# Kernel tuning notes

Hardware: AMD Instinct MI355X
Metric: run time of the kernel (lower is better)

Reference implementation:

```python
import jax, jax.numpy as jnp
import numpy as np

LEVELS = [(128, 128), (64, 64), (32, 32), (16, 16)]  # (H, W) per level
B, D, NH, NL, NP, DFF, NLAYERS = 2, 256, 8, 4, 4, 1024, 6
DH = D // NH
Q = sum(h * w for h, w in LEVELS)


def setup_inputs() -> dict:
    key = jax.random.key(0)
    ks = iter(jax.random.split(key, 64))
    inp = {}
    for i, (h, w) in enumerate(LEVELS):
        inp[f"src{i}"] = jax.random.normal(next(ks), (B, D, h, w), jnp.float32)
        inp[f"pos{i}"] = jax.random.normal(next(ks), (B, D, h, w), jnp.float32) * 0.1
    s = 0.02
    def p(shape):
        return jax.random.normal(next(ks), shape, jnp.float32) * s
    inp["level_embed"] = p((NL, D))
    inp["W_off"] = p((NLAYERS, D, NH * NL * NP * 2)); inp["b_off"] = p((NLAYERS, NH * NL * NP * 2))
    inp["W_aw"] = p((NLAYERS, D, NH * NL * NP)); inp["b_aw"] = p((NLAYERS, NH * NL * NP))
    inp["W_v"] = p((NLAYERS, D, D)); inp["b_v"] = p((NLAYERS, D))
    inp["W_out"] = p((NLAYERS, D, D)); inp["b_out"] = p((NLAYERS, D))
    inp["g1"] = jnp.ones((NLAYERS, D)); inp["be1"] = jnp.zeros((NLAYERS, D))
    inp["W1"] = p((NLAYERS, D, DFF)); inp["b1"] = p((NLAYERS, DFF))
    inp["W2"] = p((NLAYERS, DFF, D)); inp["b2"] = p((NLAYERS, D))
    inp["g2"] = jnp.ones((NLAYERS, D)); inp["be2"] = jnp.zeros((NLAYERS, D))
    return inp


def layer_norm(x, g, b, eps=1e-5):
    m = x.mean(-1, keepdims=True)
    v = ((x - m) ** 2).mean(-1, keepdims=True)
    return (x - m) * jax.lax.rsqrt(v + eps) * g + b


def bilinear_sample(v, loc, H, W):
    # v: [B,NH,H*W,DH], loc: [B,NH,Q,NP,2] normalized to [0,1] (grid_sample, align_corners=False, zero pad)
    x = loc[..., 0] * W - 0.5
    y = loc[..., 1] * H - 0.5
    x0f = jnp.floor(x); y0f = jnp.floor(y)
    wx = (x - x0f)[..., None]; wy = (y - y0f)[..., None]
    x0 = x0f.astype(jnp.int32); y0 = y0f.astype(jnp.int32)
    def gather(xi, yi):
        ok = ((xi >= 0) & (xi < W) & (yi >= 0) & (yi < H))[..., None]
        idx = jnp.clip(yi, 0, H - 1) * W + jnp.clip(xi, 0, W - 1)
        b, h, q, pp = idx.shape
        g = jnp.take_along_axis(v, idx.reshape(b, h, q * pp, 1), axis=2).reshape(b, h, q, pp, -1)
        return jnp.where(ok, g, jnp.zeros((), v.dtype))
    v00 = gather(x0, y0); v10 = gather(x0 + 1, y0)
    v01 = gather(x0, y0 + 1); v11 = gather(x0 + 1, y0 + 1)
    return (v00 * (1 - wx) * (1 - wy) + v10 * wx * (1 - wy)
            + v01 * (1 - wx) * wy + v11 * wx * wy)


def deform_attn(x, q, ref, wh, Woff, boff, Waw, baw, Wv, bv, Wout, bout):
    off = (q @ Woff + boff).reshape(B, Q, NH, NL, NP, 2)
    aw = jax.nn.softmax((q @ Waw + baw).reshape(B, Q, NH, NL * NP), -1).reshape(B, Q, NH, NL, NP)
    v = (x @ Wv + bv).reshape(B, Q, NH, DH)
    # sampling locations: [B,Q,NH,NL,NP,2]
    loc = ref[:, :, None, :, None, :] + off / wh[None, None, None, :, None, :]
    out = jnp.zeros((B, Q, NH, DH), x.dtype)
    start = 0
    for lvl, (h, w) in enumerate(LEVELS):
        n = h * w
        vl = v[:, start:start + n].transpose(0, 2, 1, 3)          # [B,NH,n,DH]
        locl = loc[:, :, :, lvl].transpose(0, 2, 1, 3, 4)          # [B,NH,Q,NP,2]
        sampled = bilinear_sample(vl, locl, h, w)                  # [B,NH,Q,NP,DH]
        out = out + jnp.einsum('bqhp,bhqpd->bqhd', aw[:, :, :, lvl], sampled)
        start += n
    return out.reshape(B, Q, D) @ Wout + bout


def _ref_points():
    refs = []
    for h, w in LEVELS:
        ry, rx = jnp.meshgrid(jnp.linspace(0.5, h - 0.5, h) / h,
                              jnp.linspace(0.5, w - 0.5, w) / w, indexing='ij')
        refs.append(jnp.stack([rx.reshape(-1), ry.reshape(-1)], -1))
    r = jnp.concatenate(refs, 0)                                   # [Q,2]
    return jnp.broadcast_to(r[None, :, None, :], (B, Q, NL, 2))    # valid_ratios == 1


def reference(src0, src1, src2, src3, pos0, pos1, pos2, pos3, level_embed,
              W_off, b_off, W_aw, b_aw, W_v, b_v, W_out, b_out,
              g1, be1, W1, b1, W2, b2, g2, be2):
    srcs = [src0, src1, src2, src3]
    poss = [pos0, pos1, pos2, pos3]
    x = jnp.concatenate([s.reshape(B, D, -1).transpose(0, 2, 1) for s in srcs], 1)
    pos = jnp.concatenate([p.reshape(B, D, -1).transpose(0, 2, 1) + level_embed[i][None, None]
                           for i, p in enumerate(poss)], 1)
    ref = _ref_points()
    wh = jnp.array([[w, h] for h, w in LEVELS], jnp.float32)       # offset normalizer (W,H)
    for l in range(NLAYERS):
        q = x + pos
        attn = deform_attn(x, q, ref, wh, W_off[l], b_off[l], W_aw[l], b_aw[l],
                           W_v[l], b_v[l], W_out[l], b_out[l])
        x = layer_norm(x + attn, g1[l], be1[l])
        f = jax.nn.relu(x @ W1[l] + b1[l]) @ W2[l] + b2[l]
        x = layer_norm(x + f, g2[l], be2[l])
    spatial_shapes = jnp.array(LEVELS, jnp.int32)
    sizes = np.array([h * w for h, w in LEVELS])
    level_start_index = jnp.array(np.concatenate([[0], np.cumsum(sizes)[:-1]]), jnp.int32)
    return (x, spatial_shapes, level_start_index)
```

## Files before the change

### kernel.cpp

```cpp
#include <hip/hip_runtime.h>
#include <cstddef>

#define BB 2
#define DD 256
#define NH 8
#define NL 4
#define NP 4
#define DFF 1024
#define NLAYERS 6
#define Q_TOT 21760
#define NTOK (BB * Q_TOT)
#define MTILES (NTOK / 128)
#define LTILES (NTOK / 64)

typedef unsigned short ushort_t;
typedef __attribute__((ext_vector_type(8))) short bh8;
typedef __attribute__((ext_vector_type(4))) float fx4;

__device__ __forceinline__ ushort_t f2b(float x) {
  union { float f; unsigned u; } v; v.f = x;
  unsigned r = v.u + 0x7FFF + ((v.u >> 16) & 1);
  return (ushort_t)(r >> 16);
}
__device__ __forceinline__ float b2f(ushort_t b) {
  union { unsigned u; float f; } v; v.u = ((unsigned)b) << 16; return v.f;
}
__device__ __forceinline__ float b2f_hi(unsigned w) {
  union { unsigned u; float f; } v; v.u = w & 0xFFFF0000u; return v.f;
}
__device__ __forceinline__ float b2f_lo(unsigned w) {
  union { unsigned u; float f; } v; v.u = w << 16; return v.f;
}

__device__ __forceinline__ void gload16(const void* g, void* l) {
  __builtin_amdgcn_global_load_lds(
      (const __attribute__((address_space(1))) unsigned int*)g,
      (__attribute__((address_space(3))) unsigned int*)l, 16, 0, 0);
}

__global__ __launch_bounds__(256) void flatten_level(
    const float* __restrict__ src, const float* __restrict__ pos,
    const float* __restrict__ lemb, float* __restrict__ X,
    ushort_t* __restrict__ Xb, ushort_t* __restrict__ POSb,
    ushort_t* __restrict__ QBb, int HW, int start, int lvl) {
  __shared__ float ts[32][33];
  __shared__ float tp[32][33];
  int p0 = blockIdx.x * 32, d0 = blockIdx.y * 32, b = blockIdx.z;
  const float* sb = src + (size_t)b * DD * HW;
  const float* pb = pos + (size_t)b * DD * HW;
  int px = threadIdx.x;
#pragma unroll
  for (int i = 0; i < 4; ++i) {
    int dl = threadIdx.y + i * 8;
    ts[dl][px] = sb[(size_t)(d0 + dl) * HW + p0 + px];
    tp[dl][px] = pb[(size_t)(d0 + dl) * HW + p0 + px];
  }
  __syncthreads();
  int dx = threadIdx.x;
#pragma unroll
  for (int i = 0; i < 4; ++i) {
    int pl = threadIdx.y + i * 8;
    size_t row = (size_t)b * Q_TOT + start + p0 + pl;
    float s = ts[dx][pl];
    float p = tp[dx][pl] + lemb[lvl * DD + d0 + dx];
    X[row * DD + d0 + dx] = s;
    Xb[row * DD + d0 + dx] = f2b(s);
    POSb[row * DD + d0 + dx] = f2b(p);
    QBb[row * DD + d0 + dx] = f2b(s + p);
  }
}

__global__ __launch_bounds__(256) void transpose_w(const float* __restrict__ W,
                                                   ushort_t* __restrict__ WT,
                                                   int K, int N, int outStride,
                                                   int rowOff) {
  __shared__ float t[32][33];
  int n0 = blockIdx.x * 32, k0 = blockIdx.y * 32, l = blockIdx.z;
  const float* in = W + (size_t)l * K * N;
  ushort_t* out = WT + (size_t)l * outStride;
#pragma unroll
  for (int i = 0; i < 4; ++i) {
    int k = threadIdx.y + i * 8;
    t[k][threadIdx.x] = in[(size_t)(k0 + k) * N + n0 + threadIdx.x];
  }
  __syncthreads();
#pragma unroll
  for (int i = 0; i < 4; ++i) {
    int nn = threadIdx.y + i * 8;
    out[(size_t)(rowOff + n0 + nn) * K + k0 + threadIdx.x] = f2b(t[threadIdx.x][nn]);
  }
}

__global__ void pack_bias(const float* __restrict__ b_off,
                          const float* __restrict__ b_aw,
                          float* __restrict__ b_qa) {
  int l = blockIdx.x, i = threadIdx.x;
  b_qa[l * 384 + i] = (i < 256) ? b_off[l * 256 + i] : b_aw[l * 128 + i - 256];
}

template <int RELU, int OUTBF16>
__global__ __launch_bounds__(256) void gemm_mfma(
    const ushort_t* __restrict__ A, const ushort_t* __restrict__ Bt,
    const float* __restrict__ bias, void* __restrict__ C, int N, int K) {
  __shared__ ushort_t As[128 * 64];
  __shared__ ushort_t Bs[128 * 64];
  int tid = threadIdx.x;
  int m0 = blockIdx.y * 128, n0 = blockIdx.x * 128;
  int wid = tid >> 6, lane = tid & 63;
  int wr = wid >> 1, wc = wid & 1;

  fx4 acc[4][4];
#pragma unroll
  for (int i = 0; i < 4; ++i)
#pragma unroll
    for (int j = 0; j < 4; ++j) acc[i][j] = fx4{0.f, 0.f, 0.f, 0.f};

  const ushort_t* ga = A + (size_t)(m0 + (tid >> 3)) * K + (tid & 7) * 8;
  const ushort_t* gb = Bt + (size_t)(n0 + (tid >> 3)) * K + (tid & 7) * 8;
  int ldsbase = wid * 1024;

  for (int k0 = 0; k0 < K; k0 += 64) {
#pragma unroll
    for (int it = 0; it < 4; ++it) {
      gload16(ga + (size_t)(it * 32) * K + k0, (char*)As + ldsbase + it * 4096);
      gload16(gb + (size_t)(it * 32) * K + k0, (char*)Bs + ldsbase + it * 4096);
    }
    __syncthreads();
#pragma unroll
    for (int kk = 0; kk < 2; ++kk) {
      bh8 af[4], bf[4];
      int cb = kk * 64 + (lane >> 4) * 16;
      int ra = wr * 64 + (lane & 15);
      int rb = wc * 64 + (lane & 15);
#pragma unroll
      for (int i = 0; i < 4; ++i)
        af[i] = *(const bh8*)((const char*)As + (ra + i * 16) * 128 + cb);
#pragma unroll
      for (int i = 0; i < 4; ++i)
        bf[i] = *(const bh8*)((const char*)Bs + (rb + i * 16) * 128 + cb);
#pragma unroll
      for (int i = 0; i < 4; ++i)
#pragma unroll
        for (int j = 0; j < 4; ++j)
          acc[i][j] = __builtin_amdgcn_mfma_f32_16x16x32_bf16(af[i], bf[j], acc[i][j], 0, 0, 0);
    }
    __syncthreads();
  }

  int crow = m0 + wr * 64 + (lane >> 4) * 4;
  int ccol = n0 + wc * 64 + (lane & 15);
#pragma unroll
  for (int j = 0; j < 4; ++j) {
    float bv = bias[ccol + j * 16];
#pragma unroll
    for (int i = 0; i < 4; ++i) {
#pragma unroll
      for (int r = 0; r < 4; ++r) {
        float v = acc[i][j][r] + bv;
        if (RELU) v = fmaxf(v, 0.f);
        size_t idx = (size_t)(crow + i * 16 + r) * N + ccol + j * 16;
        if (OUTBF16) ((ushort_t*)C)[idx] = f2b(v);
        else ((float*)C)[idx] = v;
      }
    }
  }
}

__global__ __launch_bounds__(256) void gemm_ln(
    const ushort_t* __restrict__ A, const ushort_t* __restrict__ Bt,
    const float* __restrict__ bias, const float* __restrict__ gamma,
    const float* __restrict__ beta, ushort_t* __restrict__ Xbio, int K) {
  __shared__ ushort_t As[2][64 * 32];
  __shared__ ushort_t Bs[2][256 * 32];
  __shared__ float red[2][2][64];
  int tid = threadIdx.x;
  int m0 = blockIdx.x * 64;
  int wid = tid >> 6, lane = tid & 63;
  int wr = wid >> 1, wc = wid & 1;

  fx4 acc[2][8];
#pragma unroll
  for (int i = 0; i < 2; ++i)
#pragma unroll
    for (int j = 0; j < 8; ++j) acc[i][j] = fx4{0.f, 0.f, 0.f, 0.f};

  int srow = tid >> 2;
  int sslot = (tid & 3) ^ ((tid >> 3) & 3);
  const ushort_t* ga = A + (size_t)(m0 + srow) * K + sslot * 8;
  const ushort_t* gb = Bt + (size_t)srow * K + sslot * 8;
  int ldsoff = wid * 1024;

  int cbyte = (((lane >> 4) ^ ((lane >> 1) & 3)) << 4);
  int ra = wr * 32 + (lane & 15);
  int rb = wc * 128 + (lane & 15);

  gload16(ga, (char*)As[0] + ldsoff);
#pragma unroll
  for (int it = 0; it < 4; ++it)
    gload16(gb + (size_t)(it * 64) * K, (char*)Bs[0] + it * 4096 + ldsoff);
  __syncthreads();

  int nt = K >> 5;
  int cur = 0;
  for (int t = 0; t < nt; ++t) {
    if (t + 1 < nt) {
      int k1 = (t + 1) << 5;
      gload16(ga + k1, (char*)As[cur ^ 1] + ldsoff);
#pragma unroll
      for (int it = 0; it < 4; ++it)
        gload16(gb + (size_t)(it * 64) * K + k1, (char*)Bs[cur ^ 1] + it * 4096 + ldsoff);
    }
    bh8 af[2], bf[8];
#pragma unroll
    for (int i = 0; i < 2; ++i)
      af[i] = *(const bh8*)((const char*)As[cur] + (ra + i * 16) * 64 + cbyte);
#pragma unroll
    for (int j = 0; j < 8; ++j)
      bf[j] = *(const bh8*)((const char*)Bs[cur] + (rb + j * 16) * 64 + cbyte);
#pragma unroll
    for (int i = 0; i < 2; ++i)
#pragma unroll
      for (int j = 0; j < 8; ++j)
        acc[i][j] = __builtin_amdgcn_mfma_f32_16x16x32_bf16(af[i], bf[j], acc[i][j], 0, 0, 0);
    __syncthreads();
    cur ^= 1;
  }

  int lg = lane >> 4, lc = lane & 15;
  float bv[8], gv[8], bev[8];
#pragma unroll
  for (int j = 0; j < 8; ++j) {
    int col = wc * 128 + j * 16 + lc;
    bv[j] = bias[col];
    gv[j] = gamma[col];
    bev[j] = beta[col];
  }
#pragma unroll
  for (int i = 0; i < 2; ++i) {
#pragma unroll
    for (int r = 0; r < 4; ++r) {
      int rloc = wr * 32 + i * 16 + lg * 4 + r;
      const ushort_t* xr = Xbio + (size_t)(m0 + rloc) * DD + wc * 128 + lc;
      float s = 0.f, s2 = 0.f;
#pragma unroll
      for (int j = 0; j < 8; ++j) {
        float v = acc[i][j][r] + bv[j] + b2f(xr[j * 16]);
        acc[i][j][r] = v;
        s += v;
        s2 += v * v;
      }
#pragma unroll
      for (int o = 1; o < 16; o <<= 1) {
        s += __shfl_xor(s, o);
        s2 += __shfl_xor(s2, o);
      }
      if (lc == 0) {
        red[wc][0][rloc] = s;
        red[wc][1][rloc] = s2;
      }
    }
  }
  __syncthreads();
#pragma unroll
  for (int i = 0; i < 2; ++i) {
#pragma unroll
    for (int r = 0; r < 4; ++r) {
      int rloc = wr * 32 + i * 16 + lg * 4 + r;
      float s = red[0][0][rloc] + red[1][0][rloc];
      float s2 = red[0][1][rloc] + red[1][1][rloc];
      float mmean = s * (1.f / 256.f);
      float var = s2 * (1.f / 256.f) - mmean * mmean;
      float inv = rsqrtf(var + 1e-5f);
      size_t rowb = (size_t)(m0 + rloc) * DD + wc * 128 + lc;
#pragma unroll
      for (int j = 0; j < 8; ++j) {
        float y = (acc[i][j][r] - mmean) * inv * gv[j] + bev[j];
        Xbio[rowb + j * 16] = f2b(y);
      }
    }
  }
}

template <int LAST>
__global__ __launch_bounds__(512, 2) void ffn_fused(
    const ushort_t* __restrict__ Xio, const ushort_t* __restrict__ W1t,
    const float* __restrict__ b1v, const ushort_t* __restrict__ W2t,
    const float* __restrict__ b2v, const float* __restrict__ gamma,
    const float* __restrict__ beta, const ushort_t* __restrict__ POSb,
    ushort_t* __restrict__ QBb, float* __restrict__ Xf) {
  extern __shared__ char lds[];
  int tid = threadIdx.x;
  int w = tid >> 6, l = tid & 63;
  int l15 = l & 15, l4 = l >> 4, l7 = l & 7;
  int m0 = blockIdx.x * 64;

  fx4 acc[4][8];
#pragma unroll
  for (int i = 0; i < 4; ++i)
#pragma unroll
    for (int j = 0; j < 8; ++j) acc[i][j] = fx4{0.f, 0.f, 0.f, 0.f};

  const ushort_t* xb = Xio + (size_t)m0 * 256;
#pragma unroll
  for (int kk = 0; kk < 8; ++kk) {
    bh8 af[4], bf[8];
#pragma unroll
    for (int i = 0; i < 4; ++i)
      af[i] = *(const bh8*)(xb + (size_t)(l15 + 16 * i) * 256 + kk * 32 + l4 * 8);
#pragma unroll
    for (int j = 0; j < 8; ++j)
      bf[j] = *(const bh8*)(W1t + (size_t)(w * 128 + j * 16 + l15) * 256 + kk * 32 + l4 * 8);
#pragma unroll
    for (int i = 0; i < 4; ++i)
#pragma unroll
      for (int j = 0; j < 8; ++j)
        acc[i][j] = __builtin_amdgcn_mfma_f32_16x16x32_bf16(af[i], bf[j], acc[i][j], 0, 0, 0);
  }
#pragma unroll
  for (int j = 0; j < 8; ++j) {
    int n = w * 128 + j * 16 + l15;
    float bb = b1v[n];
    int slotbase = n >> 3;
    int nlo = (n & 7) * 2;
#pragma unroll
    for (int i = 0; i < 4; ++i) {
#pragma unroll
      for (int r = 0; r < 4; ++r) {
        int m = l4 * 4 + r + 16 * i;
        float h = fmaxf(acc[i][j][r] + bb, 0.f);
        *(ushort_t*)(lds + m * 2048 + ((slotbase ^ (m & 7)) << 4) + nlo) = f2b(h);
      }
    }
  }
  __syncthreads();

  fx4 acc2[4][2];
#pragma unroll
  for (int i = 0; i < 4; ++i)
#pragma unroll
    for (int j = 0; j < 2; ++j) acc2[i][j] = fx4{0.f, 0.f, 0.f, 0.f};

#pragma unroll 4
  for (int kt = 0; kt < 32; ++kt) {
    bh8 af[4], bf[2];
#pragma unroll
    for (int i = 0; i < 4; ++i) {
      int m = l15 + 16 * i;
      af[i] = *(const bh8*)(lds + m * 2048 + (((kt * 4 + l4) ^ l7) << 4));
    }
#pragma unroll
    for (int j = 0; j < 2; ++j)
      bf[j] = *(const bh8*)(W2t + (size_t)(w * 32 + j * 16 + l15) * 1024 + kt * 32 + l4 * 8);
#pragma unroll
    for (int i = 0; i < 4; ++i)
#pragma unroll
      for (int j = 0; j < 2; ++j)
        acc2[i][j] = __builtin_amdgcn_mfma_f32_16x16x32_bf16(af[i], bf[j], acc2[i][j], 0, 0, 0);
  }
  __syncthreads();

  float* red = (float*)lds;
  float* minv = (float*)(lds + 4096);

  float gv[2], bev[2], bv2[2];
#pragma unroll
  for (int j = 0; j < 2; ++j) {
    int col = w * 32 + j * 16 + l15;
    gv[j] = gamma[col];
    bev[j] = beta[col];
    bv2[j] = b2v[col];
  }
#pragma unroll
  for (int i = 0; i < 4; ++i) {
#pragma unroll
    for (int r = 0; r < 4; ++r) {
      int m = l4 * 4 + r + 16 * i;
      float s = 0.f, s2 = 0.f;
#pragma unroll
      for (int j = 0; j < 2; ++j) {
        int col = w * 32 + j * 16 + l15;
        float v = acc2[i][j][r] + bv2[j] + b2f(Xio[(size_t)(m0 + m) * 256 + col]);
        acc2[i][j][r] = v;
        s += v;
        s2 += v * v;
      }
#pragma unroll
      for (int o = 1; o < 16; o <<= 1) {
        s += __shfl_xor(s, o);
        s2 += __shfl_xor(s2, o);
      }
      if (l15 == 0) {
        red[w * 64 + m] = s;
        red[512 + w * 64 + m] = s2;
      }
    }
  }
  __syncthreads();
  if (tid < 64) {
    float s = 0.f, s2 = 0.f;
#pragma unroll
    for (int ww = 0; ww < 8; ++ww) {
      s += red[ww * 64 + tid];
      s2 += red[512 + ww * 64 + tid];
    }
    float mean = s * (1.f / 256.f);
    float var = s2 * (1.f / 256.f) - mean * mean;
    minv[tid * 2] = mean;
    minv[tid * 2 + 1] = rsqrtf(var + 1e-5f);
  }
  __syncthreads();
  ushort_t* XbOut = (ushort_t*)Xio;
#pragma unroll
  for (int i = 0; i < 4; ++i) {
#pragma unroll
    for (int r = 0; r < 4; ++r) {
      int m = l4 * 4 + r + 16 * i;
      float mean = minv[m * 2], inv = minv[m * 2 + 1];
      size_t rowb = (size_t)(m0 + m) * 256;
#pragma unroll
      for (int j = 0; j < 2; ++j) {
        int col = w * 32 + j * 16 + l15;
        float y = (acc2[i][j][r] - mean) * inv * gv[j] + bev[j];
        XbOut[rowb + col] = f2b(y);
        if (LAST) Xf[rowb + col] = y;
        else QBb[rowb + col] = f2b(y + b2f(POSb[rowb + col]));
      }
    }
  }
}

__global__ __launch_bounds__(256) void sample_v4(const ushort_t* __restrict__ Vb,
                                                 const ushort_t* __restrict__ QA,
                                                 ushort_t* __restrict__ SAMPb) {
  int nb = NTOK / 2;
  int bid = blockIdx.x;
  int newb = (bid & 7) * (nb >> 3) + (bid >> 3);
  int t = newb * 2 + (threadIdx.x >> 7);
  int h = (threadIdx.x >> 4) & 7;
  int p = threadIdx.x & 15;

  int b = (t >= Q_TOT) ? 1 : 0;
  int qi = t - b * Q_TOT;
  int lwq = (qi < 16384) ? 7 : (qi < 20480) ? 6 : (qi < 21504) ? 5 : 4;
  int stq = (qi < 16384) ? 0 : (qi < 20480) ? 16384 : (qi < 21504) ? 20480 : 21504;
  int wt = 1 << lwq;
  int pidx = qi - stq;
  int iy = pidx >> lwq, ix = pidx & (wt - 1);
  float refx = (ix + 0.5f) / (float)wt;
  float refy = (iy + 0.5f) / (float)wt;

  float lgt = b2f(QA[(size_t)t * 384 + 256 + h * 16 + p]);
  float mxv = lgt;
#pragma unroll
  for (int o = 1; o < 16; o <<= 1) mxv = fmaxf(mxv, __shfl_xor(mxv, o, 16));
  float e = __expf(lgt - mxv);
  float sum = e;
#pragma unroll
  for (int o = 1; o < 16; o <<= 1) sum += __shfl_xor(sum, o, 16);
  float a = e / sum;

  int l = p >> 2, pt = p & 3;
  int wl = 128 >> l;
  int LSl = (l > 0 ? 16384 : 0) + (l > 1 ? 4096 : 0) + (l > 2 ? 1024 : 0);
  float fw = (float)wl;
  unsigned ow = *(const unsigned*)(QA + (size_t)t * 384 + h * 32 + l * 8 + pt * 2);
  float ox = b2f_lo(ow), oy = b2f_hi(ow);
  float Xc = refx * fw + ox - 0.5f;
  float Yc = refy * fw + oy - 0.5f;
  float xf = floorf(Xc), yf = floorf(Yc);
  float wx = Xc - xf, wy = Yc - yf;
  int x0 = (int)xf, y0 = (int)yf;
  int x1 = x0 + 1, y1 = y0 + 1;
  float ok_x0 = (x0 >= 0 && x0 < wl) ? 1.f : 0.f;
  float ok_x1 = (x1 >= 0 && x1 < wl) ? 1.f : 0.f;
  float ok_y0 = (y0 >= 0 && y0 < wl) ? 1.f : 0.f;
  float ok_y1 = (y1 >= 0 && y1 < wl) ? 1.f : 0.f;
  int xc0 = min(max(x0, 0), wl - 1), xc1 = min(max(x1, 0), wl - 1);
  int yc0 = min(max(y0, 0), wl - 1), yc1 = min(max(y1, 0), wl - 1);
  float w00 = (1.f - wx) * (1.f - wy) * a * ok_x0 * ok_y0;
  float w10 = wx * (1.f - wy) * a * ok_x1 * ok_y0;
  float w01 = (1.f - wx) * wy * a * ok_x0 * ok_y1;
  float w11 = wx * wy * a * ok_x1 * ok_y1;
  int metaBase = ((b * Q_TOT + LSl + yc0 * wl + xc0) << 8) + h * 32;
  int metaDxy = (int)(((unsigned)((xc1 - xc0) << 8)) |
                      (((unsigned)((yc1 - yc0) * wl) << 8) << 16));
  int metaZ = (int)(((unsigned)f2b(w00) << 16) | f2b(w10));
  int metaW = (int)(((unsigned)f2b(w01) << 16) | f2b(w11));

  int c2 = p * 2;
  float acc0 = 0.f, acc1 = 0.f;
#pragma unroll
  for (int pp = 0; pp < 16; ++pp) {
    int m0v = __shfl(metaBase, pp, 16);
    int m1v = __shfl(metaDxy, pp, 16);
    int mzv = __shfl(metaZ, pp, 16);
    int mwv = __shfl(metaW, pp, 16);
    unsigned dxy = (unsigned)m1v;
    int base = m0v + c2;
    int dx = (int)(dxy & 0xffffu);
    int dy = (int)(dxy >> 16);
    unsigned v00 = *(const unsigned*)(Vb + base);
    unsigned v10 = *(const unsigned*)(Vb + base + dx);
    unsigned v01 = *(const unsigned*)(Vb + base + dy);
    unsigned v11 = *(const unsigned*)(Vb + base + dy + dx);
    unsigned wz = (unsigned)mzv, ww = (unsigned)mwv;
    float f00 = b2f_hi(wz), f10 = b2f_lo(wz);
    float f01 = b2f_hi(ww), f11 = b2f_lo(ww);
    acc0 = fmaf(f00, b2f_lo(v00), acc0);
    acc1 = fmaf(f00, b2f_hi(v00), acc1);
    acc0 = fmaf(f10, b2f_lo(v10), acc0);
    acc1 = fmaf(f10, b2f_hi(v10), acc1);
    acc0 = fmaf(f01, b2f_lo(v01), acc0);
    acc1 = fmaf(f01, b2f_hi(v01), acc1);
    acc0 = fmaf(f11, b2f_lo(v11), acc0);
    acc1 = fmaf(f11, b2f_hi(v11), acc1);
  }
  unsigned outw = (unsigned)f2b(acc0) | ((unsigned)f2b(acc1) << 16);
  *(unsigned*)(SAMPb + (size_t)t * 256 + h * 32 + c2) = outw;
}

__global__ void write_tail(float* __restrict__ t) {
  int i = threadIdx.x;
  float v = 0.f;
  switch (i) {
    case 0: v = 128.f; break;
    case 1: v = 128.f; break;
    case 2: v = 64.f; break;
    case 3: v = 64.f; break;
    case 4: v = 32.f; break;
    case 5: v = 32.f; break;
    case 6: v = 16.f; break;
    case 7: v = 16.f; break;
    case 8: v = 0.f; break;
    case 9: v = 16384.f; break;
    case 10: v = 20480.f; break;
    case 11: v = 21504.f; break;
    default: return;
  }
  t[i] = v;
}

extern "C" void kernel_launch(void* const* d_in, const int* in_sizes, int n_in,
                              void* d_out, int out_size, void* d_ws, size_t ws_size,
                              hipStream_t stream) {
  const float* src[4] = {(const float*)d_in[0], (const float*)d_in[2],
                         (const float*)d_in[4], (const float*)d_in[6]};
  const float* pos[4] = {(const float*)d_in[1], (const float*)d_in[3],
                         (const float*)d_in[5], (const float*)d_in[7]};
  const float* lemb = (const float*)d_in[8];
  const float* W_off = (const float*)d_in[9];
  const float* b_off = (const float*)d_in[10];
  const float* W_aw = (const float*)d_in[11];
  const float* b_aw = (const float*)d_in[12];
  const float* W_v = (const float*)d_in[13];
  const float* b_v = (const float*)d_in[14];
  const float* W_out = (const float*)d_in[15];
  const float* b_out = (const float*)d_in[16];
  const float* g1 = (const float*)d_in[17];
  const float* be1 = (const float*)d_in[18];
  const float* W1 = (const float*)d_in[19];
  const float* b1 = (const float*)d_in[20];
  const float* W2 = (const float*)d_in[21];
  const float* b2 = (const float*)d_in[22];
  const float* g2 = (const float*)d_in[23];
  const float* be2 = (const float*)d_in[24];

  float* X = (float*)d_out;

  char* w = (char*)d_ws;
  const size_t SZ_B = (size_t)NTOK * 256 * 2;
  ushort_t* POSb = (ushort_t*)w;  w += SZ_B;
  ushort_t* Xb = (ushort_t*)w;    w += SZ_B;
  ushort_t* QBb = (ushort_t*)w;   w += SZ_B;
  ushort_t* QAb = (ushort_t*)w;   w += (size_t)NTOK * 384 * 2;
  ushort_t* Vb = (ushort_t*)w;    w += SZ_B;
  ushort_t* SAMPb = (ushort_t*)w; w += SZ_B;
  ushort_t* WT_qa = (ushort_t*)w;  w += (size_t)NLAYERS * 384 * 256 * 2;
  ushort_t* WT_v = (ushort_t*)w;   w += (size_t)NLAYERS * 256 * 256 * 2;
  ushort_t* WT_out = (ushort_t*)w; w += (size_t)NLAYERS * 256 * 256 * 2;
  ushort_t* WT_1 = (ushort_t*)w;   w += (size_t)NLAYERS * 1024 * 256 * 2;
  ushort_t* WT_2 = (ushort_t*)w;   w += (size_t)NLAYERS * 256 * 1024 * 2;
  float* b_qa = (float*)w;         w += (size_t)NLAYERS * 384 * 4;

  hipFuncSetAttribute((const void*)ffn_fused<0>,
                      hipFuncAttributeMaxDynamicSharedMemorySize, 131072);
  hipFuncSetAttribute((const void*)ffn_fused<1>,
                      hipFuncAttributeMaxDynamicSharedMemorySize, 131072);

  transpose_w<<<dim3(8, 8, NLAYERS), dim3(32, 8), 0, stream>>>(W_off, WT_qa, 256, 256, 384 * 256, 0);
  transpose_w<<<dim3(4, 8, NLAYERS), dim3(32, 8), 0, stream>>>(W_aw, WT_qa, 256, 128, 384 * 256, 256);
  pack_bias<<<NLAYERS, 384, 0, stream>>>(b_off, b_aw, b_qa);
  transpose_w<<<dim3(8, 8, NLAYERS), dim3(32, 8), 0, stream>>>(W_v, WT_v, 256, 256, 256 * 256, 0);
  transpose_w<<<dim3(8, 8, NLAYERS), dim3(32, 8), 0, stream>>>(W_out, WT_out, 256, 256, 256 * 256, 0);
  transpose_w<<<dim3(32, 8, NLAYERS), dim3(32, 8), 0, stream>>>(W1, WT_1, 256, 1024, 1024 * 256, 0);
  transpose_w<<<dim3(8, 32, NLAYERS), dim3(32, 8), 0, stream>>>(W2, WT_2, 1024, 256, 256 * 1024, 0);

  static const int LWh[4] = {128, 64, 32, 16};
  static const int LSh[4] = {0, 16384, 20480, 21504};
  for (int l = 0; l < 4; ++l) {
    int hw = LWh[l] * LWh[l];
    dim3 g(hw / 32, DD / 32, BB);
    flatten_level<<<g, dim3(32, 8), 0, stream>>>(src[l], pos[l], lemb, X, Xb, POSb,
                                                 QBb, hw, LSh[l], l);
  }
  write_tail<<<1, 16, 0, stream>>>(X + (size_t)NTOK * DD);

  for (int l = 0; l < NLAYERS; ++l) {
    gemm_mfma<0, 1><<<dim3(3, MTILES), 256, 0, stream>>>(
        QBb, WT_qa + (size_t)l * 384 * 256, b_qa + l * 384, QAb, 384, 256);
    gemm_mfma<0, 1><<<dim3(2, MTILES), 256, 0, stream>>>(
        Xb, WT_v + (size_t)l * 256 * 256, b_v + l * 256, Vb, 256, 256);
    sample_v4<<<NTOK / 2, 256, 0, stream>>>(Vb, QAb, SAMPb);
    gemm_ln<<<LTILES, 256, 0, stream>>>(
        SAMPb, WT_out + (size_t)l * 256 * 256, b_out + l * 256,
        g1 + l * DD, be1 + l * DD, Xb, 256);
    if (l + 1 < NLAYERS) {
      ffn_fused<0><<<LTILES, 512, 131072, stream>>>(
          Xb, WT_1 + (size_t)l * 1024 * 256, b1 + l * DFF,
          WT_2 + (size_t)l * 256 * 1024, b2 + l * 256,
          g2 + l * DD, be2 + l * DD, POSb, QBb, X);
    } else {
      ffn_fused<1><<<LTILES, 512, 131072, stream>>>(
          Xb, WT_1 + (size_t)l * 1024 * 256, b1 + l * DFF,
          WT_2 + (size_t)l * 256 * 1024, b2 + l * 256,
          g2 + l * DD, be2 + l * DD, POSb, QBb, X);
    }
  }
}
```

Baseline: 1.846 ms.

## Shrink FFN tile to 32 rows, stage X in LDS, raise occupancy

The fused FFN kernel now processes 32 tokens per block instead of 64. The X tile is staged once into swizzled LDS through gload16, and that copy serves both the first GEMM's A operand and the residual read. The first GEMM is split into two 64-column subchunks to reduce accumulator registers, LDS drops to 80KB, and launch bounds ask for more resident blocks. The goal is higher occupancy and less redundant global traffic, at the cost of twice as many W1/W2 reads from global/L2 per token.

```diff
diff --git a/kernel.cpp b/kernel.cpp
--- a/kernel.cpp
+++ b/kernel.cpp
@@ -12,6 +12,7 @@
 #define NTOK (BB * Q_TOT)
 #define MTILES (NTOK / 128)
 #define LTILES (NTOK / 64)
+#define FTILES (NTOK / 32)
 
 typedef unsigned short ushort_t;
 typedef __attribute__((ext_vector_type(8))) short bh8;
@@ -282,7 +283,7 @@
 }
 
 template <int LAST>
-__global__ __launch_bounds__(512, 2) void ffn_fused(
+__global__ __launch_bounds__(512, 4) void ffn_fused(
     const ushort_t* __restrict__ Xio, const ushort_t* __restrict__ W1t,
     const float* __restrict__ b1v, const ushort_t* __restrict__ W2t,
     const float* __restrict__ b2v, const float* __restrict__ gamma,
@@ -291,68 +292,84 @@
   extern __shared__ char lds[];
   int tid = threadIdx.x;
   int w = tid >> 6, l = tid & 63;
-  int l15 = l & 15, l4 = l >> 4, l7 = l & 7;
-  int m0 = blockIdx.x * 64;
-
-  fx4 acc[4][8];
-#pragma unroll
-  for (int i = 0; i < 4; ++i)
-#pragma unroll
-    for (int j = 0; j < 8; ++j) acc[i][j] = fx4{0.f, 0.f, 0.f, 0.f};
-
-  const ushort_t* xb = Xio + (size_t)m0 * 256;
-#pragma unroll
-  for (int kk = 0; kk < 8; ++kk) {
-    bh8 af[4], bf[8];
-#pragma unroll
-    for (int i = 0; i < 4; ++i)
-      af[i] = *(const bh8*)(xb + (size_t)(l15 + 16 * i) * 256 + kk * 32 + l4 * 8);
-#pragma unroll
-    for (int j = 0; j < 8; ++j)
-      bf[j] = *(const bh8*)(W1t + (size_t)(w * 128 + j * 16 + l15) * 256 + kk * 32 + l4 * 8);
-#pragma unroll
-    for (int i = 0; i < 4; ++i)
-#pragma unroll
-      for (int j = 0; j < 8; ++j)
-        acc[i][j] = __builtin_amdgcn_mfma_f32_16x16x32_bf16(af[i], bf[j], acc[i][j], 0, 0, 0);
-  }
-#pragma unroll
-  for (int j = 0; j < 8; ++j) {
-    int n = w * 128 + j * 16 + l15;
-    float bb = b1v[n];
-    int slotbase = n >> 3;
-    int nlo = (n & 7) * 2;
-#pragma unroll
-    for (int i = 0; i < 4; ++i) {
-#pragma unroll
-      for (int r = 0; r < 4; ++r) {
-        int m = l4 * 4 + r + 16 * i;
-        float h = fmaxf(acc[i][j][r] + bb, 0.f);
-        *(ushort_t*)(lds + m * 2048 + ((slotbase ^ (m & 7)) << 4) + nlo) = f2b(h);
-      }
-    }
-  }
-  __syncthreads();
-
-  fx4 acc2[4][2];
-#pragma unroll
-  for (int i = 0; i < 4; ++i)
+  int l15 = l & 15, l4 = l >> 4, l7 = l15 & 7;
+  int m0 = blockIdx.x * 32;
+
+  {
+    const ushort_t* xg = Xio + (size_t)m0 * 256;
+#pragma unroll
+    for (int it = 0; it < 2; ++it) {
+      int sl = tid + it * 512;
+      int row = sl >> 5, s = sl & 31;
+      gload16(xg + row * 256 + (s ^ (row & 7)) * 8,
+              lds + 65536 + (size_t)(w * 64 + it * 512) * 16);
+    }
+  }
+  __syncthreads();
+
+#pragma unroll
+  for (int sc = 0; sc < 2; ++sc) {
+    fx4 acc[2][4];
+#pragma unroll
+    for (int i = 0; i < 2; ++i)
+#pragma unroll
+      for (int j = 0; j < 4; ++j) acc[i][j] = fx4{0.f, 0.f, 0.f, 0.f};
+#pragma unroll
+    for (int kk = 0; kk < 8; ++kk) {
+      bh8 af[2], bf[4];
+#pragma unroll
+      for (int i = 0; i < 2; ++i) {
+        int m = i * 16 + l15;
+        af[i] = *(const bh8*)(lds + 65536 + m * 512 + (((kk * 4 + l4) ^ l7) << 4));
+      }
+#pragma unroll
+      for (int j = 0; j < 4; ++j)
+        bf[j] = *(const bh8*)(W1t + (size_t)(w * 128 + sc * 64 + j * 16 + l15) * 256 +
+                              kk * 32 + l4 * 8);
+#pragma unroll
+      for (int i = 0; i < 2; ++i)
+#pragma unroll
+        for (int j = 0; j < 4; ++j)
+          acc[i][j] = __builtin_amdgcn_mfma_f32_16x16x32_bf16(af[i], bf[j], acc[i][j], 0, 0, 0);
+    }
+#pragma unroll
+    for (int j = 0; j < 4; ++j) {
+      int n = w * 128 + sc * 64 + j * 16 + l15;
+      float bb = b1v[n];
+      int slotbase = n >> 3;
+      int nlo = (n & 7) * 2;
+#pragma unroll
+      for (int i = 0; i < 2; ++i) {
+#pragma unroll
+        for (int r = 0; r < 4; ++r) {
+          int m = i * 16 + l4 * 4 + r;
+          float h = fmaxf(acc[i][j][r] + bb, 0.f);
+          *(ushort_t*)(lds + m * 2048 + ((slotbase ^ (m & 7)) << 4) + nlo) = f2b(h);
+        }
+      }
+    }
+  }
+  __syncthreads();
+
+  fx4 acc2[2][2];
+#pragma unroll
+  for (int i = 0; i < 2; ++i)
 #pragma unroll
     for (int j = 0; j < 2; ++j) acc2[i][j] = fx4{0.f, 0.f, 0.f, 0.f};
 
-#pragma unroll 4
+#pragma unroll 8
   for (int kt = 0; kt < 32; ++kt) {
-    bh8 af[4], bf[2];
-#pragma unroll
-    for (int i = 0; i < 4; ++i) {
-      int m = l15 + 16 * i;
-      af[i] = *(const bh8*)(lds + m * 2048 + (((kt * 4 + l4) ^ l7) << 4));
+    bh8 af[2], bf[2];
+#pragma unroll
+    for (int i = 0; i < 2; ++i) {
+      int m = i * 16 + l15;
+      af[i] = *(const bh8*)(lds + m * 2048 + (((kt * 4 + l4) ^ (m & 7)) << 4));
     }
 #pragma unroll
     for (int j = 0; j < 2; ++j)
       bf[j] = *(const bh8*)(W2t + (size_t)(w * 32 + j * 16 + l15) * 1024 + kt * 32 + l4 * 8);
 #pragma unroll
-    for (int i = 0; i < 4; ++i)
+    for (int i = 0; i < 2; ++i)
 #pragma unroll
       for (int j = 0; j < 2; ++j)
         acc2[i][j] = __builtin_amdgcn_mfma_f32_16x16x32_bf16(af[i], bf[j], acc2[i][j], 0, 0, 0);
@@ -371,15 +388,17 @@
     bv2[j] = b2v[col];
   }
 #pragma unroll
-  for (int i = 0; i < 4; ++i) {
+  for (int i = 0; i < 2; ++i) {
 #pragma unroll
     for (int r = 0; r < 4; ++r) {
-      int m = l4 * 4 + r + 16 * i;
+      int m = i * 16 + l4 * 4 + r;
       float s = 0.f, s2 = 0.f;
 #pragma unroll
       for (int j = 0; j < 2; ++j) {
-        int col = w * 32 + j * 16 + l15;
-        float v = acc2[i][j][r] + bv2[j] + b2f(Xio[(size_t)(m0 + m) * 256 + col]);
+        int n = w * 32 + j * 16 + l15;
+        float xr = b2f(*(const ushort_t*)(lds + 65536 + m * 512 +
+                                          (((n >> 3) ^ (m & 7)) << 4) + (n & 7) * 2));
+        float v = acc2[i][j][r] + bv2[j] + xr;
         acc2[i][j][r] = v;
         s += v;
         s2 += v * v;
@@ -390,18 +409,18 @@
         s2 += __shfl_xor(s2, o);
       }
       if (l15 == 0) {
-        red[w * 64 + m] = s;
-        red[512 + w * 64 + m] = s2;
-      }
-    }
-  }
-  __syncthreads();
-  if (tid < 64) {
+        red[w * 32 + m] = s;
+        red[256 + w * 32 + m] = s2;
+      }
+    }
+  }
+  __syncthreads();
+  if (tid < 32) {
     float s = 0.f, s2 = 0.f;
 #pragma unroll
     for (int ww = 0; ww < 8; ++ww) {
-      s += red[ww * 64 + tid];
-      s2 += red[512 + ww * 64 + tid];
+      s += red[ww * 32 + tid];
+      s2 += red[256 + ww * 32 + tid];
     }
     float mean = s * (1.f / 256.f);
     float var = s2 * (1.f / 256.f) - mean * mean;
@@ -411,10 +430,10 @@
   __syncthreads();
   ushort_t* XbOut = (ushort_t*)Xio;
 #pragma unroll
-  for (int i = 0; i < 4; ++i) {
+  for (int i = 0; i < 2; ++i) {
 #pragma unroll
     for (int r = 0; r < 4; ++r) {
-      int m = l4 * 4 + r + 16 * i;
+      int m = i * 16 + l4 * 4 + r;
       float mean = minv[m * 2], inv = minv[m * 2 + 1];
       size_t rowb = (size_t)(m0 + m) * 256;
 #pragma unroll
@@ -583,9 +602,9 @@
   float* b_qa = (float*)w;         w += (size_t)NLAYERS * 384 * 4;
 
   hipFuncSetAttribute((const void*)ffn_fused<0>,
-                      hipFuncAttributeMaxDynamicSharedMemorySize, 131072);
+                      hipFuncAttributeMaxDynamicSharedMemorySize, 81920);
   hipFuncSetAttribute((const void*)ffn_fused<1>,
-                      hipFuncAttributeMaxDynamicSharedMemorySize, 131072);
+                      hipFuncAttributeMaxDynamicSharedMemorySize, 81920);
 
   transpose_w<<<dim3(8, 8, NLAYERS), dim3(32, 8), 0, stream>>>(W_off, WT_qa, 256, 256, 384 * 256, 0);
   transpose_w<<<dim3(4, 8, NLAYERS), dim3(32, 8), 0, stream>>>(W_aw, WT_qa, 256, 128, 384 * 256, 256);
@@ -615,12 +634,12 @@
         SAMPb, WT_out + (size_t)l * 256 * 256, b_out + l * 256,
         g1 + l * DD, be1 + l * DD, Xb, 256);
     if (l + 1 < NLAYERS) {
-      ffn_fused<0><<<LTILES, 512, 131072, stream>>>(
+      ffn_fused<0><<<FTILES, 512, 81920, stream>>>(
           Xb, WT_1 + (size_t)l * 1024 * 256, b1 + l * DFF,
           WT_2 + (size_t)l * 256 * 1024, b2 + l * 256,
           g2 + l * DD, be2 + l * DD, POSb, QBb, X);
     } else {
-      ffn_fused<1><<<LTILES, 512, 131072, stream>>>(
+      ffn_fused<1><<<FTILES, 512, 81920, stream>>>(
           Xb, WT_1 + (size_t)l * 1024 * 256, b1 + l * DFF,
           WT_2 + (size_t)l * 256 * 1024, b2 + l * 256,
           g2 + l * DD, be2 + l * DD, POSb, QBb, X);
```

Measured after the change: 2.040 ms. 1.11x slower.

## Chunk FFN hidden dimension to shrink LDS and registers for higher occupancy

Applied to the files above, without the earlier changes.

The fused FFN kernel now processes the 1024-wide hidden layer in eight 128-column chunks. Each chunk's ReLU output is staged in a small padded static LDS buffer and immediately consumed by the second GEMM, replacing the 128 KB dynamic LDS tile and the large first-GEMM accumulator array. Launch bounds are raised so more blocks can be resident per CU, aiming to hide latency. In exchange it adds two barriers per chunk and reloads the X tile from global/cache for every chunk.

```diff
diff --git a/kernel.cpp b/kernel.cpp
--- a/kernel.cpp
+++ b/kernel.cpp
@@ -282,85 +282,75 @@
 }
 
 template <int LAST>
-__global__ __launch_bounds__(512, 2) void ffn_fused(
+__global__ __launch_bounds__(512, 4) void ffn_fused(
     const ushort_t* __restrict__ Xio, const ushort_t* __restrict__ W1t,
     const float* __restrict__ b1v, const ushort_t* __restrict__ W2t,
     const float* __restrict__ b2v, const float* __restrict__ gamma,
     const float* __restrict__ beta, const ushort_t* __restrict__ POSb,
     ushort_t* __restrict__ QBb, float* __restrict__ Xf) {
-  extern __shared__ char lds[];
+  __shared__ ushort_t Hs[64 * 136];
+  __shared__ float red[1024];
+  __shared__ float minv[128];
   int tid = threadIdx.x;
   int w = tid >> 6, l = tid & 63;
-  int l15 = l & 15, l4 = l >> 4, l7 = l & 7;
+  int l15 = l & 15, l4 = l >> 4;
   int m0 = blockIdx.x * 64;
 
-  fx4 acc[4][8];
+  const ushort_t* xb = Xio + (size_t)m0 * 256;
+
+  fx4 acc2[4][2];
 #pragma unroll
   for (int i = 0; i < 4; ++i)
 #pragma unroll
-    for (int j = 0; j < 8; ++j) acc[i][j] = fx4{0.f, 0.f, 0.f, 0.f};
-
-  const ushort_t* xb = Xio + (size_t)m0 * 256;
-#pragma unroll
-  for (int kk = 0; kk < 8; ++kk) {
-    bh8 af[4], bf[8];
-#pragma unroll
-    for (int i = 0; i < 4; ++i)
-      af[i] = *(const bh8*)(xb + (size_t)(l15 + 16 * i) * 256 + kk * 32 + l4 * 8);
-#pragma unroll
-    for (int j = 0; j < 8; ++j)
-      bf[j] = *(const bh8*)(W1t + (size_t)(w * 128 + j * 16 + l15) * 256 + kk * 32 + l4 * 8);
-#pragma unroll
-    for (int i = 0; i < 4; ++i)
-#pragma unroll
-      for (int j = 0; j < 8; ++j)
-        acc[i][j] = __builtin_amdgcn_mfma_f32_16x16x32_bf16(af[i], bf[j], acc[i][j], 0, 0, 0);
-  }
-#pragma unroll
-  for (int j = 0; j < 8; ++j) {
-    int n = w * 128 + j * 16 + l15;
-    float bb = b1v[n];
-    int slotbase = n >> 3;
-    int nlo = (n & 7) * 2;
-#pragma unroll
-    for (int i = 0; i < 4; ++i) {
-#pragma unroll
-      for (int r = 0; r < 4; ++r) {
-        int m = l4 * 4 + r + 16 * i;
-        float h = fmaxf(acc[i][j][r] + bb, 0.f);
-        *(ushort_t*)(lds + m * 2048 + ((slotbase ^ (m & 7)) << 4) + nlo) = f2b(h);
-      }
-    }
-  }
-  __syncthreads();
-
-  fx4 acc2[4][2];
-#pragma unroll
-  for (int i = 0; i < 4; ++i)
-#pragma unroll
     for (int j = 0; j < 2; ++j) acc2[i][j] = fx4{0.f, 0.f, 0.f, 0.f};
 
-#pragma unroll 4
-  for (int kt = 0; kt < 32; ++kt) {
-    bh8 af[4], bf[2];
-#pragma unroll
-    for (int i = 0; i < 4; ++i) {
-      int m = l15 + 16 * i;
-      af[i] = *(const bh8*)(lds + m * 2048 + (((kt * 4 + l4) ^ l7) << 4));
-    }
-#pragma unroll
-    for (int j = 0; j < 2; ++j)
-      bf[j] = *(const bh8*)(W2t + (size_t)(w * 32 + j * 16 + l15) * 1024 + kt * 32 + l4 * 8);
-#pragma unroll
-    for (int i = 0; i < 4; ++i)
+#pragma unroll 1
+  for (int c = 0; c < 8; ++c) {
+    fx4 acc1[4];
+#pragma unroll
+    for (int i = 0; i < 4; ++i) acc1[i] = fx4{0.f, 0.f, 0.f, 0.f};
+#pragma unroll
+    for (int kk = 0; kk < 8; ++kk) {
+      bh8 af[4], bf;
+#pragma unroll
+      for (int i = 0; i < 4; ++i)
+        af[i] = *(const bh8*)(xb + (size_t)(i * 16 + l15) * 256 + kk * 32 + l4 * 8);
+      bf = *(const bh8*)(W1t + (size_t)(c * 128 + w * 16 + l15) * 256 + kk * 32 + l4 * 8);
+#pragma unroll
+      for (int i = 0; i < 4; ++i)
+        acc1[i] = __builtin_amdgcn_mfma_f32_16x16x32_bf16(af[i], bf, acc1[i], 0, 0, 0);
+    }
+    {
+      int n = w * 16 + l15;
+      float bb = b1v[c * 128 + n];
+#pragma unroll
+      for (int i = 0; i < 4; ++i) {
+#pragma unroll
+        for (int r = 0; r < 4; ++r) {
+          int m = i * 16 + l4 * 4 + r;
+          Hs[m * 136 + n] = f2b(fmaxf(acc1[i][r] + bb, 0.f));
+        }
+      }
+    }
+    __syncthreads();
+#pragma unroll
+    for (int kt = 0; kt < 4; ++kt) {
+      bh8 af[4], bf[2];
+#pragma unroll
+      for (int i = 0; i < 4; ++i)
+        af[i] = *(const bh8*)(Hs + (size_t)(i * 16 + l15) * 136 + kt * 32 + l4 * 8);
 #pragma unroll
       for (int j = 0; j < 2; ++j)
-        acc2[i][j] = __builtin_amdgcn_mfma_f32_16x16x32_bf16(af[i], bf[j], acc2[i][j], 0, 0, 0);
-  }
-  __syncthreads();
-
-  float* red = (float*)lds;
-  float* minv = (float*)(lds + 4096);
+        bf[j] = *(const bh8*)(W2t + (size_t)(w * 32 + j * 16 + l15) * 1024 +
+                              c * 128 + kt * 32 + l4 * 8);
+#pragma unroll
+      for (int i = 0; i < 4; ++i)
+#pragma unroll
+        for (int j = 0; j < 2; ++j)
+          acc2[i][j] = __builtin_amdgcn_mfma_f32_16x16x32_bf16(af[i], bf[j], acc2[i][j], 0, 0, 0);
+    }
+    __syncthreads();
+  }
 
   float gv[2], bev[2], bv2[2];
 #pragma unroll
@@ -582,11 +572,6 @@
   ushort_t* WT_2 = (ushort_t*)w;   w += (size_t)NLAYERS * 256 * 1024 * 2;
   float* b_qa = (float*)w;         w += (size_t)NLAYERS * 384 * 4;
 
-  hipFuncSetAttribute((const void*)ffn_fused<0>,
-                      hipFuncAttributeMaxDynamicSharedMemorySize, 131072);
-  hipFuncSetAttribute((const void*)ffn_fused<1>,
-                      hipFuncAttributeMaxDynamicSharedMemorySize, 131072);
-
   transpose_w<<<dim3(8, 8, NLAYERS), dim3(32, 8), 0, stream>>>(W_off, WT_qa, 256, 256, 384 * 256, 0);
   transpose_w<<<dim3(4, 8, NLAYERS), dim3(32, 8), 0, stream>>>(W_aw, WT_qa, 256, 128, 384 * 256, 256);
   pack_bias<<<NLAYERS, 384, 0, stream>>>(b_off, b_aw, b_qa);
@@ -615,12 +600,12 @@
         SAMPb, WT_out + (size_t)l * 256 * 256, b_out + l * 256,
         g1 + l * DD, be1 + l * DD, Xb, 256);
     if (l + 1 < NLAYERS) {
-      ffn_fused<0><<<LTILES, 512, 131072, stream>>>(
+      ffn_fused<0><<<LTILES, 512, 0, stream>>>(
           Xb, WT_1 + (size_t)l * 1024 * 256, b1 + l * DFF,
           WT_2 + (size_t)l * 256 * 1024, b2 + l * 256,
           g2 + l * DD, be2 + l * DD, POSb, QBb, X);
     } else {
-      ffn_fused<1><<<LTILES, 512, 131072, stream>>>(
+      ffn_fused<1><<<LTILES, 512, 0, stream>>>(
           Xb, WT_1 + (size_t)l * 1024 * 256, b1 + l * DFF,
           WT_2 + (size_t)l * 256 * 1024, b2 + l * 256,
           g2 + l * DD, be2 + l * DD, POSb, QBb, X);
```

After: 2.672 ms. +44.8%, slower.

## Use FP8 for FFN second GEMM with halved LDS hidden buffer

Applied to the files above, without the earlier changes.

Stores the FFN hidden activations in LDS as FP8 and pre-converts W2 to scaled FP8, so the second GEMM runs on fp8 MFMA with a 1/16 rescale in the epilogue. Halving the LDS footprint to 64KB and raising launch bounds to 4 blocks per CU is meant to increase occupancy. The first GEMM is split into two column halves to cut accumulator registers. This lowers the precision of the FFN hidden activations and W2, which risks accuracy tolerance failures.

```diff
diff --git a/kernel.cpp b/kernel.cpp
--- a/kernel.cpp
+++ b/kernel.cpp
@@ -91,6 +91,28 @@
   }
 }
 
+__global__ __launch_bounds__(256) void transpose_w_fp8(const float* __restrict__ W,
+                                                       unsigned char* __restrict__ WT,
+                                                       int K, int N, float scale) {
+  __shared__ float t[32][33];
+  int n0 = blockIdx.x * 32, k0 = blockIdx.y * 32, l = blockIdx.z;
+  const float* in = W + (size_t)l * K * N;
+  unsigned char* out = WT + (size_t)l * N * K;
+#pragma unroll
+  for (int i = 0; i < 4; ++i) {
+    int k = threadIdx.y + i * 8;
+    t[k][threadIdx.x] = in[(size_t)(k0 + k) * N + n0 + threadIdx.x];
+  }
+  __syncthreads();
+#pragma unroll
+  for (int i = 0; i < 4; ++i) {
+    int nn = threadIdx.y + i * 8;
+    float v = t[threadIdx.x][nn] * scale;
+    int p = __builtin_amdgcn_cvt_pk_fp8_f32(v, 0.f, 0, false);
+    out[(size_t)(n0 + nn) * K + k0 + threadIdx.x] = (unsigned char)(p & 0xFF);
+  }
+}
+
 __global__ void pack_bias(const float* __restrict__ b_off,
                           const float* __restrict__ b_aw,
                           float* __restrict__ b_qa) {
@@ -282,53 +304,59 @@
 }
 
 template <int LAST>
-__global__ __launch_bounds__(512, 2) void ffn_fused(
+__global__ __launch_bounds__(512, 4) void ffn_fused(
     const ushort_t* __restrict__ Xio, const ushort_t* __restrict__ W1t,
-    const float* __restrict__ b1v, const ushort_t* __restrict__ W2t,
+    const float* __restrict__ b1v, const unsigned char* __restrict__ W2f8,
     const float* __restrict__ b2v, const float* __restrict__ gamma,
     const float* __restrict__ beta, const ushort_t* __restrict__ POSb,
     ushort_t* __restrict__ QBb, float* __restrict__ Xf) {
   extern __shared__ char lds[];
   int tid = threadIdx.x;
   int w = tid >> 6, l = tid & 63;
-  int l15 = l & 15, l4 = l >> 4, l7 = l & 7;
+  int l15 = l & 15, l4 = l >> 4;
   int m0 = blockIdx.x * 64;
 
-  fx4 acc[4][8];
-#pragma unroll
-  for (int i = 0; i < 4; ++i)
-#pragma unroll
-    for (int j = 0; j < 8; ++j) acc[i][j] = fx4{0.f, 0.f, 0.f, 0.f};
-
   const ushort_t* xb = Xio + (size_t)m0 * 256;
-#pragma unroll
-  for (int kk = 0; kk < 8; ++kk) {
-    bh8 af[4], bf[8];
+
+#pragma unroll
+  for (int sc = 0; sc < 2; ++sc) {
+    fx4 acc1[4][4];
 #pragma unroll
     for (int i = 0; i < 4; ++i)
-      af[i] = *(const bh8*)(xb + (size_t)(l15 + 16 * i) * 256 + kk * 32 + l4 * 8);
-#pragma unroll
-    for (int j = 0; j < 8; ++j)
-      bf[j] = *(const bh8*)(W1t + (size_t)(w * 128 + j * 16 + l15) * 256 + kk * 32 + l4 * 8);
-#pragma unroll
-    for (int i = 0; i < 4; ++i)
-#pragma unroll
-      for (int j = 0; j < 8; ++j)
-        acc[i][j] = __builtin_amdgcn_mfma_f32_16x16x32_bf16(af[i], bf[j], acc[i][j], 0, 0, 0);
-  }
-#pragma unroll
-  for (int j = 0; j < 8; ++j) {
-    int n = w * 128 + j * 16 + l15;
-    float bb = b1v[n];
-    int slotbase = n >> 3;
-    int nlo = (n & 7) * 2;
-#pragma unroll
-    for (int i = 0; i < 4; ++i) {
-#pragma unroll
-      for (int r = 0; r < 4; ++r) {
-        int m = l4 * 4 + r + 16 * i;
-        float h = fmaxf(acc[i][j][r] + bb, 0.f);
-        *(ushort_t*)(lds + m * 2048 + ((slotbase ^ (m & 7)) << 4) + nlo) = f2b(h);
+#pragma unroll
+      for (int j = 0; j < 4; ++j) acc1[i][j] = fx4{0.f, 0.f, 0.f, 0.f};
+#pragma unroll
+    for (int kk = 0; kk < 8; ++kk) {
+      bh8 af[4], bf[4];
+#pragma unroll
+      for (int i = 0; i < 4; ++i)
+        af[i] = *(const bh8*)(xb + (size_t)(l15 + 16 * i) * 256 + kk * 32 + l4 * 8);
+#pragma unroll
+      for (int j = 0; j < 4; ++j)
+        bf[j] = *(const bh8*)(W1t + (size_t)(w * 128 + sc * 64 + j * 16 + l15) * 256 +
+                              kk * 32 + l4 * 8);
+#pragma unroll
+      for (int i = 0; i < 4; ++i)
+#pragma unroll
+        for (int j = 0; j < 4; ++j)
+          acc1[i][j] = __builtin_amdgcn_mfma_f32_16x16x32_bf16(bf[j], af[i], acc1[i][j], 0, 0, 0);
+    }
+#pragma unroll
+    for (int j = 0; j < 4; ++j) {
+      int n0 = w * 128 + sc * 64 + j * 16 + l4 * 4;
+      float4 bb4 = *(const float4*)(b1v + n0);
+      int slot = n0 >> 4;
+      int inner = l4 * 4;
+#pragma unroll
+      for (int i = 0; i < 4; ++i) {
+        int m = i * 16 + l15;
+        float h0 = fmaxf(acc1[i][j][0] + bb4.x, 0.f);
+        float h1 = fmaxf(acc1[i][j][1] + bb4.y, 0.f);
+        float h2 = fmaxf(acc1[i][j][2] + bb4.z, 0.f);
+        float h3 = fmaxf(acc1[i][j][3] + bb4.w, 0.f);
+        int d = __builtin_amdgcn_cvt_pk_fp8_f32(h0, h1, 0, false);
+        d = __builtin_amdgcn_cvt_pk_fp8_f32(h2, h3, d, true);
+        *(int*)(lds + m * 1024 + ((slot ^ (m & 7)) << 4) + inner) = d;
       }
     }
   }
@@ -342,20 +370,21 @@
 
 #pragma unroll 4
   for (int kt = 0; kt < 32; ++kt) {
-    bh8 af[4], bf[2];
+    long aL[4], bL[2];
 #pragma unroll
     for (int i = 0; i < 4; ++i) {
-      int m = l15 + 16 * i;
-      af[i] = *(const bh8*)(lds + m * 2048 + (((kt * 4 + l4) ^ l7) << 4));
+      int m = i * 16 + l15;
+      int slot = kt * 2 + (l4 >> 1);
+      aL[i] = *(const long*)(lds + m * 1024 + ((slot ^ (m & 7)) << 4) + (l4 & 1) * 8);
     }
 #pragma unroll
     for (int j = 0; j < 2; ++j)
-      bf[j] = *(const bh8*)(W2t + (size_t)(w * 32 + j * 16 + l15) * 1024 + kt * 32 + l4 * 8);
+      bL[j] = *(const long*)(W2f8 + (size_t)(w * 32 + j * 16 + l15) * 1024 + kt * 32 + l4 * 8);
 #pragma unroll
     for (int i = 0; i < 4; ++i)
 #pragma unroll
       for (int j = 0; j < 2; ++j)
-        acc2[i][j] = __builtin_amdgcn_mfma_f32_16x16x32_bf16(af[i], bf[j], acc2[i][j], 0, 0, 0);
+        acc2[i][j] = __builtin_amdgcn_mfma_f32_16x16x32_fp8_fp8(aL[i], bL[j], acc2[i][j], 0, 0, 0);
   }
   __syncthreads();
 
@@ -379,7 +408,7 @@
 #pragma unroll
       for (int j = 0; j < 2; ++j) {
         int col = w * 32 + j * 16 + l15;
-        float v = acc2[i][j][r] + bv2[j] + b2f(Xio[(size_t)(m0 + m) * 256 + col]);
+        float v = acc2[i][j][r] * 0.0625f + bv2[j] + b2f(Xio[(size_t)(m0 + m) * 256 + col]);
         acc2[i][j][r] = v;
         s += v;
         s2 += v * v;
@@ -579,13 +608,13 @@
   ushort_t* WT_v = (ushort_t*)w;   w += (size_t)NLAYERS * 256 * 256 * 2;
   ushort_t* WT_out = (ushort_t*)w; w += (size_t)NLAYERS * 256 * 256 * 2;
   ushort_t* WT_1 = (ushort_t*)w;   w += (size_t)NLAYERS * 1024 * 256 * 2;
-  ushort_t* WT_2 = (ushort_t*)w;   w += (size_t)NLAYERS * 256 * 1024 * 2;
+  unsigned char* WT_2f8 = (unsigned char*)w; w += (size_t)NLAYERS * 256 * 1024;
   float* b_qa = (float*)w;         w += (size_t)NLAYERS * 384 * 4;
 
   hipFuncSetAttribute((const void*)ffn_fused<0>,
-                      hipFuncAttributeMaxDynamicSharedMemorySize, 131072);
+                      hipFuncAttributeMaxDynamicSharedMemorySize, 65536);
   hipFuncSetAttribute((const void*)ffn_fused<1>,
-                      hipFuncAttributeMaxDynamicSharedMemorySize, 131072);
+                      hipFuncAttributeMaxDynamicSharedMemorySize, 65536);
 
   transpose_w<<<dim3(8, 8, NLAYERS), dim3(32, 8), 0, stream>>>(W_off, WT_qa, 256, 256, 384 * 256, 0);
   transpose_w<<<dim3(4, 8, NLAYERS), dim3(32, 8), 0, stream>>>(W_aw, WT_qa, 256, 128, 384 * 256, 256);
@@ -593,7 +622,7 @@
   transpose_w<<<dim3(8, 8, NLAYERS), dim3(32, 8), 0, stream>>>(W_v, WT_v, 256, 256, 256 * 256, 0);
   transpose_w<<<dim3(8, 8, NLAYERS), dim3(32, 8), 0, stream>>>(W_out, WT_out, 256, 256, 256 * 256, 0);
   transpose_w<<<dim3(32, 8, NLAYERS), dim3(32, 8), 0, stream>>>(W1, WT_1, 256, 1024, 1024 * 256, 0);
-  transpose_w<<<dim3(8, 32, NLAYERS), dim3(32, 8), 0, stream>>>(W2, WT_2, 1024, 256, 256 * 1024, 0);
+  transpose_w_fp8<<<dim3(8, 32, NLAYERS), dim3(32, 8), 0, stream>>>(W2, WT_2f8, 1024, 256, 16.f);
 
   static const int LWh[4] = {128, 64, 32, 16};
   static const int LSh[4] = {0, 16384, 20480, 21504};
@@ -615,14 +644,14 @@
         SAMPb, WT_out + (size_t)l * 256 * 256, b_out + l * 256,
         g1 + l * DD, be1 + l * DD, Xb, 256);
     if (l + 1 < NLAYERS) {
-      ffn_fused<0><<<LTILES, 512, 131072, stream>>>(
+      ffn_fused<0><<<LTILES, 512, 65536, stream>>>(
           Xb, WT_1 + (size_t)l * 1024 * 256, b1 + l * DFF,
-          WT_2 + (size_t)l * 256 * 1024, b2 + l * 256,
+          WT_2f8 + (size_t)l * 256 * 1024, b2 + l * 256,
           g2 + l * DD, be2 + l * DD, POSb, QBb, X);
     } else {
-      ffn_fused<1><<<LTILES, 512, 131072, stream>>>(
+      ffn_fused<1><<<LTILES, 512, 65536, stream>>>(
           Xb, WT_1 + (size_t)l * 1024 * 256, b1 + l * DFF,
-          WT_2 + (size_t)l * 256 * 1024, b2 + l * 256,
+          WT_2f8 + (size_t)l * 256 * 1024, b2 + l * 256,
           g2 + l * DD, be2 + l * DD, POSb, QBb, X);
     }
   }
```

Result: slower. 2.004 ms (+8.6%).
